# Kernel tuning notes

Hardware: AMD Instinct MI355X
Metric: run time of the kernel (lower is better)

Reference implementation:

```python
import jax, jax.numpy as jnp
import numpy as np

K = 5            # neighbors
TEMP = 1.0       # softmax temperature
BANK = 1000      # fixed bank capacity in source
B = 65536        # batch
D = 256          # feature_dim
EPS = 1e-12      # F.normalize eps


def _l2norm(x):
    # F.normalize(x, dim=1): x / max(||x||, eps)
    n = jnp.sqrt(jnp.sum(x * x, axis=1, keepdims=True))
    return x / jnp.maximum(n, EPS)


def setup_inputs() -> dict:
    key = jax.random.key(0)
    k1, k2, k3, k4 = jax.random.split(key, 4)
    features = jax.random.normal(k1, (B, D), dtype=jnp.float32)
    feature_bank = jax.random.normal(k2, (BANK, D), dtype=jnp.float32)
    # fusion_layer: Linear(2D -> D), ReLU, Linear(D -> D). torch weight layout [out, in].
    W1 = jax.random.normal(k3, (D, 2 * D), dtype=jnp.float32) * (1.0 / np.sqrt(2 * D))
    b1 = jnp.zeros((D,), dtype=jnp.float32)
    W2 = jax.random.normal(k4, (D, D), dtype=jnp.float32) * (1.0 / np.sqrt(D))
    b2 = jnp.zeros((D,), dtype=jnp.float32)
    return {"features": features, "feature_bank": feature_bank,
            "W1": W1, "b1": b1, "W2": W2, "b2": b2}


def reference(features, feature_bank, W1, b1, W2, b2):
    # knn_search: cosine similarity against the (full) bank
    qn = _l2norm(features)                      # [B, D]
    bn = _l2norm(feature_bank)                  # [BANK, D]
    sims = qn @ bn.T                            # [B, BANK]
    top_s, top_i = jax.lax.top_k(sims, K)       # [B, K]
    w = jax.nn.softmax(top_s / TEMP, axis=1)    # [B, K]
    neigh = feature_bank[top_i]                 # gather -> [B, K, D]
    nf = jnp.einsum('bkd,bk->bd', neigh, w)     # weighted average of neighbors
    # fusion MLP on concat([query, neighbors])
    fused = jnp.concatenate([features, nf], axis=1)    # [B, 2D]
    h = jax.nn.relu(fused @ W1.T + b1)                 # [B, D]
    out = h @ W2.T + b2                                # [B, D]
    return out
```

## Files before the change

kernel.cpp:

```cpp
#include <hip/hip_runtime.h>

#define DIM 256
#define NC 12

typedef __attribute__((ext_vector_type(8))) short short8;
typedef __attribute__((ext_vector_type(4))) float f32x4;

__device__ __forceinline__ short f32bf(float f) {
    unsigned u = __builtin_bit_cast(unsigned, f);
    unsigned r = u + 0x7FFFu + ((u >> 16) & 1u);
    return (short)(r >> 16);
}

template<int CTRL>
__device__ __forceinline__ unsigned dppmax(unsigned x) {
    unsigned y = (unsigned)__builtin_amdgcn_update_dpp(0, (int)x, CTRL, 0xF, 0xF, true);
    return x > y ? x : y;
}

__global__ __launch_bounds__(256) void k_prep(const float* __restrict__ bank,
        const float* __restrict__ W1, const float* __restrict__ W2,
        short* __restrict__ bnbf, double* __restrict__ binv,
        short* __restrict__ w1bf, short* __restrict__ w2bf)
{
    __shared__ double part[4];
    __shared__ double s_inv;
    const int bid = blockIdx.x, t = threadIdx.x;
    if (bid < 1024) {
        const int row = bid;
        if (row < 1000) {
            float v = bank[(size_t)row * DIM + t];
            double ssq = (double)v * (double)v;
            for (int o = 32; o > 0; o >>= 1) ssq += __shfl_down(ssq, o);
            if ((t & 63) == 0) part[t >> 6] = ssq;
            __syncthreads();
            if (t == 0) {
                double s = part[0] + part[1] + part[2] + part[3];
                double n = sqrt(s); if (n < 1e-12) n = 1e-12;
                double inv = 1.0 / n;
                binv[row] = inv; s_inv = inv;
            }
            __syncthreads();
            bnbf[(size_t)row * DIM + t] = f32bf((float)((double)v * s_inv));
        } else {
            bnbf[(size_t)row * DIM + t] = 0;
            if (t == 0) binv[row] = 0.0;
        }
    } else if (bid < 1536) {
        const int i = (bid - 1024) * 256 + t;
        w1bf[i] = f32bf(W1[i]);
    } else {
        const int i = (bid - 1536) * 256 + t;
        w2bf[i] = f32bf(W2[i]);
    }
}

__global__ __launch_bounds__(256) void k_sims(const float* __restrict__ feat,
        const short* __restrict__ bnbf, int* __restrict__ top)
{
    __shared__ alignas(16) short S[32 * 1032];
    const int t = threadIdx.x, lane = t & 63, w = t >> 6;
    const int n16 = lane & 15, q4 = lane >> 4;
    const int qb = blockIdx.x * 32;

    short8 bq[8][2];
    #pragma unroll
    for (int kc = 0; kc < 8; ++kc)
        #pragma unroll
        for (int nt = 0; nt < 2; ++nt) {
            const float4* s = (const float4*)(feat + (size_t)(qb + nt * 16 + n16) * DIM + kc * 32 + q4 * 8);
            float4 v0 = s[0], v1 = s[1];
            short8 f;
            f[0] = f32bf(v0.x); f[1] = f32bf(v0.y); f[2] = f32bf(v0.z); f[3] = f32bf(v0.w);
            f[4] = f32bf(v1.x); f[5] = f32bf(v1.y); f[6] = f32bf(v1.z); f[7] = f32bf(v1.w);
            bq[kc][nt] = f;
        }

    const char* Abase = (const char*)bnbf + ((size_t)(w * 16 + n16) * DIM + q4 * 8) * 2;
    const f32x4 vzero = {0.f, 0.f, 0.f, 0.f};

    short8 A[3][8];
    #pragma unroll
    for (int kc = 0; kc < 8; ++kc) A[0][kc] = *(const short8*)(Abase + kc * 64);
    #pragma unroll
    for (int kc = 0; kc < 8; ++kc) A[1][kc] = *(const short8*)(Abase + 32768 + kc * 64);

    #pragma unroll
    for (int chunk = 0; chunk < 16; ++chunk) {
        if (chunk + 2 < 16) {
            const char* nb = Abase + (size_t)(chunk + 2) * 32768;
            #pragma unroll
            for (int kc = 0; kc < 8; ++kc)
                A[(chunk + 2) % 3][kc] = *(const short8*)(nb + kc * 64);
        }
        f32x4 acc0 = vzero, acc1 = vzero;
        #pragma unroll
        for (int kc = 0; kc < 8; ++kc) {
            acc0 = __builtin_amdgcn_mfma_f32_16x16x32_bf16(A[chunk % 3][kc], bq[kc][0], acc0, 0, 0, 0);
            acc1 = __builtin_amdgcn_mfma_f32_16x16x32_bf16(A[chunk % 3][kc], bq[kc][1], acc1, 0, 0, 0);
        }
        const int bankb = chunk * 64 + w * 16 + q4 * 4;
        {
            uint2 u;
            u.x = ((unsigned)(unsigned short)f32bf(acc0[0])) |
                  (((unsigned)(unsigned short)f32bf(acc0[1])) << 16);
            u.y = ((unsigned)(unsigned short)f32bf(acc0[2])) |
                  (((unsigned)(unsigned short)f32bf(acc0[3])) << 16);
            *(uint2*)(S + (size_t)n16 * 1032 + bankb) = u;
            u.x = ((unsigned)(unsigned short)f32bf(acc1[0])) |
                  (((unsigned)(unsigned short)f32bf(acc1[1])) << 16);
            u.y = ((unsigned)(unsigned short)f32bf(acc1[2])) |
                  (((unsigned)(unsigned short)f32bf(acc1[3])) << 16);
            *(uint2*)(S + (size_t)(16 + n16) * 1032 + bankb) = u;
        }
    }
    __syncthreads();

    for (int i = 0; i < 8; ++i) {
        const int ql = w * 8 + i;
        const uint4* p = (const uint4*)(S + (size_t)ql * 1032 + lane * 16);
        uint4 a = p[0], b = p[1];

        unsigned k[16];
        {
            unsigned words[8] = {a.x, a.y, a.z, a.w, b.x, b.y, b.z, b.w};
            #pragma unroll
            for (int j = 0; j < 16; ++j) {
                unsigned h = (j & 1) ? (words[j >> 1] >> 16) : (words[j >> 1] & 0xFFFFu);
                unsigned m = (h ^ 0x8000u) ^ ((0u - (h >> 15)) & 0x7FFFu);
                int idx = lane * 16 + j;
                k[j] = (idx < 1000) ? ((m << 16) | (unsigned)idx) : 0u;
            }
        }
        #pragma unroll
        for (int sz = 2; sz <= 16; sz <<= 1)
            #pragma unroll
            for (int st = sz >> 1; st >= 1; st >>= 1)
                #pragma unroll
                for (int ii = 0; ii < 16; ++ii) {
                    int j = ii ^ st;
                    if (j > ii) {
                        bool desc = ((ii & sz) == 0);
                        unsigned lo = k[ii], hi = k[j];
                        unsigned mx = lo > hi ? lo : hi;
                        unsigned mn = lo > hi ? hi : lo;
                        k[ii] = desc ? mx : mn;
                        k[j] = desc ? mn : mx;
                    }
                }
        unsigned mine = 0;
        #pragma unroll
        for (int r = 0; r < 12; ++r) {
            unsigned m = k[0];
            m = dppmax<0xB1>(m);
            m = dppmax<0x4E>(m);
            m = dppmax<0x141>(m);
            m = dppmax<0x140>(m);
            m = dppmax<0x142>(m);
            m = dppmax<0x143>(m);
            unsigned wm = (unsigned)__builtin_amdgcn_readlane((int)m, 63);
            if (lane == r) mine = wm;
            if (k[0] == wm) {
                #pragma unroll
                for (int s = 0; s < 12; ++s) k[s] = k[s + 1];
            }
        }
        if (lane < 12) top[(size_t)(qb + ql) * NC + lane] = (int)(mine & 0xFFFFu);
    }
}

__global__ __launch_bounds__(256) void k_refine(const float* __restrict__ feat,
        const float* __restrict__ bank, const int* __restrict__ top,
        const double* __restrict__ binv, short* __restrict__ nf,
        short* __restrict__ featbf)
{
    __shared__ int    cidxL[16 * NC];
    __shared__ float  bdF[16 * NC];
    __shared__ double bdD[16 * NC];
    __shared__ float  simsF[16 * NC];
    __shared__ double simsD[16 * NC];
    __shared__ float  qiL[16];
    __shared__ int    flagL[16];
    __shared__ int    selidx[16][5];
    __shared__ float  selw[16][5];

    const int t = threadIdx.x, lane = t & 63, w = t >> 6;
    const int g = lane >> 4, u = lane & 15;
    const int ql = w * 4 + g;
    const int qbase = blockIdx.x * 16;
    const int q = qbase + ql;

    if (t < 16 * NC) {
        const int c = top[(size_t)qbase * NC + t];
        cidxL[t] = c;
        const double b = binv[c];
        bdD[t] = b; bdF[t] = (float)b;
    }
    __syncthreads();

    int ci[NC];
    #pragma unroll
    for (int c = 0; c < NC; ++c) ci[c] = cidxL[ql * NC + c];

    float qf[16];
    float ssf = 0.f;
    #pragma unroll
    for (int j = 0; j < 4; ++j) {
        float4 v = *(const float4*)(feat + (size_t)q * DIM + j * 64 + u * 4);
        qf[j*4+0] = v.x; qf[j*4+1] = v.y; qf[j*4+2] = v.z; qf[j*4+3] = v.w;
        ssf += v.x*v.x + v.y*v.y + v.z*v.z + v.w*v.w;
    }
    {
        short* fb = featbf + (size_t)q * DIM + u * 4;
        #pragma unroll
        for (int j = 0; j < 4; ++j) {
            uint2 pk;
            pk.x = ((unsigned)(unsigned short)f32bf(qf[j*4+0])) |
                   (((unsigned)(unsigned short)f32bf(qf[j*4+1])) << 16);
            pk.y = ((unsigned)(unsigned short)f32bf(qf[j*4+2])) |
                   (((unsigned)(unsigned short)f32bf(qf[j*4+3])) << 16);
            *(uint2*)(fb + j * 64) = pk;
        }
    }
    #pragma unroll
    for (int o = 1; o < 16; o <<= 1) ssf += __shfl_xor(ssf, o, 16);
    float nq = sqrtf(ssf); if (nq < 1e-12f) nq = 1e-12f;
    if (u == 0) qiL[ql] = 1.f / nq;

    float s[NC];
    #pragma unroll
    for (int c = 0; c < NC; ++c) {
        const float* brow = bank + (size_t)ci[c] * DIM + u * 4;
        float a0 = 0.f, a1 = 0.f, a2 = 0.f, a3 = 0.f;
        #pragma unroll
        for (int j = 0; j < 4; ++j) {
            float4 b = *(const float4*)(brow + j * 64);
            a0 += qf[j*4+0] * b.x; a1 += qf[j*4+1] * b.y;
            a2 += qf[j*4+2] * b.z; a3 += qf[j*4+3] * b.w;
        }
        s[c] = (a0 + a1) + (a2 + a3);
    }
    #pragma unroll
    for (int o = 1; o < 16; o <<= 1)
        #pragma unroll
        for (int c = 0; c < NC; ++c) s[c] += __shfl_xor(s[c], o, 16);
    #pragma unroll
    for (int c = 0; c < NC; ++c) if (u == c) simsF[ql * NC + c] = s[c];
    __syncthreads();

    if (t < 16) {
        const float qi2 = qiL[t];
        float vf[NC];
        unsigned long long key[NC];
        int cid[NC];
        #pragma unroll
        for (int c = 0; c < NC; ++c) {
            cid[c] = cidxL[t * NC + c];
            float v = simsF[t * NC + c] * qi2 * bdF[t * NC + c];
            vf[c] = v;
            unsigned ub = __builtin_bit_cast(unsigned, v);
            unsigned m = (ub >> 31) ? ~ub : (ub | 0x80000000u);
            key[c] = ((unsigned long long)m << 10) | (unsigned long long)(1023 - cid[c]);
        }
        int rank[NC];
        #pragma unroll
        for (int c = 0; c < NC; ++c) rank[c] = 0;
        #pragma unroll
        for (int c1 = 0; c1 < NC; ++c1)
            #pragma unroll
            for (int c2 = c1 + 1; c2 < NC; ++c2) {
                const bool gt = key[c1] > key[c2];
                rank[c2] += gt ? 1 : 0;
                rank[c1] += gt ? 0 : 1;
            }
        float v5 = 0.f, v6 = 0.f;
        #pragma unroll
        for (int c = 0; c < NC; ++c) {
            v5 += (rank[c] == 4) ? vf[c] : 0.f;
            v6 += (rank[c] == 5) ? vf[c] : 0.f;
        }
        flagL[t] = (v5 - v6) < 2e-6f;

        float vm = vf[0];
        #pragma unroll
        for (int c = 1; c < NC; ++c) vm = fmaxf(vm, vf[c]);
        float e[NC]; float wsum = 0.f;
        #pragma unroll
        for (int c = 0; c < NC; ++c) {
            float ex = __expf(vf[c] - vm);
            ex = (rank[c] < 5) ? ex : 0.f;
            e[c] = ex; wsum += ex;
        }
        const float inv = 1.f / wsum;
        #pragma unroll
        for (int k = 0; k < 5; ++k) {
            int idx = 0; float wv = 0.f;
            #pragma unroll
            for (int c = 0; c < NC; ++c) {
                const bool is = (rank[c] == k);
                idx += is ? cid[c] : 0;
                wv  += is ? e[c]  : 0.f;
            }
            selidx[t][k] = idx; selw[t][k] = wv * inv;
        }
    }
    __syncthreads();

    if (flagL[ql]) {
        double ssd = 0.0;
        #pragma unroll
        for (int j = 0; j < 16; ++j) ssd += (double)qf[j] * (double)qf[j];
        #pragma unroll
        for (int o = 1; o < 16; o <<= 1) ssd += __shfl_xor(ssd, o, 16);
        double nd = sqrt(ssd); if (nd < 1e-12) nd = 1e-12;
        const double qid = 1.0 / nd;
        double sd[NC];
        #pragma unroll
        for (int c = 0; c < NC; ++c) {
            const float* brow = bank + (size_t)ci[c] * DIM + u * 4;
            double a0 = 0, a1 = 0, a2 = 0, a3 = 0;
            #pragma unroll
            for (int j = 0; j < 4; ++j) {
                float4 b = *(const float4*)(brow + j * 64);
                a0 += (double)qf[j*4+0] * b.x; a1 += (double)qf[j*4+1] * b.y;
                a2 += (double)qf[j*4+2] * b.z; a3 += (double)qf[j*4+3] * b.w;
            }
            sd[c] = (a0 + a1) + (a2 + a3);
        }
        #pragma unroll
        for (int o = 1; o < 16; o <<= 1)
            #pragma unroll
            for (int c = 0; c < NC; ++c) sd[c] += __shfl_xor(sd[c], o, 16);
        #pragma unroll
        for (int c = 0; c < NC; ++c)
            if (u == c) simsD[ql * NC + c] = sd[c] * qid * bdD[ql * NC + c];
    }
    __syncthreads();

    if (t < 16 && flagL[t]) {
        double vd[NC];
        unsigned long long key[NC];
        int cid[NC];
        #pragma unroll
        for (int c = 0; c < NC; ++c) {
            cid[c] = cidxL[t * NC + c];
            double v = simsD[t * NC + c];
            vd[c] = v;
            unsigned long long ub = __builtin_bit_cast(unsigned long long, v);
            unsigned long long m = (ub >> 63) ? ~ub : (ub | 0x8000000000000000ULL);
            key[c] = (m & ~0x3FFULL) | (unsigned long long)(1023 - cid[c]);
        }
        int rank[NC];
        #pragma unroll
        for (int c = 0; c < NC; ++c) rank[c] = 0;
        #pragma unroll
        for (int c1 = 0; c1 < NC; ++c1)
            #pragma unroll
            for (int c2 = c1 + 1; c2 < NC; ++c2) {
                const bool gt = key[c1] > key[c2];
                rank[c2] += gt ? 1 : 0;
                rank[c1] += gt ? 0 : 1;
            }
        float vf[NC];
        #pragma unroll
        for (int c = 0; c < NC; ++c) vf[c] = (float)vd[c];
        float vm = vf[0];
        #pragma unroll
        for (int c = 1; c < NC; ++c) vm = fmaxf(vm, vf[c]);
        float e[NC]; float wsum = 0.f;
        #pragma unroll
        for (int c = 0; c < NC; ++c) {
            float ex = __expf(vf[c] - vm);
            ex = (rank[c] < 5) ? ex : 0.f;
            e[c] = ex; wsum += ex;
        }
        const float inv = 1.f / wsum;
        #pragma unroll
        for (int k = 0; k < 5; ++k) {
            int idx = 0; float wv = 0.f;
            #pragma unroll
            for (int c = 0; c < NC; ++c) {
                const bool is = (rank[c] == k);
                idx += is ? cid[c] : 0;
                wv  += is ? e[c]  : 0.f;
            }
            selidx[t][k] = idx; selw[t][k] = wv * inv;
        }
    }
    __syncthreads();

    float wk[5]; int ik[5];
    #pragma unroll
    for (int k = 0; k < 5; ++k) { wk[k] = selw[ql][k]; ik[k] = selidx[ql][k]; }
    float4 oa[4];
    #pragma unroll
    for (int j = 0; j < 4; ++j) { oa[j].x = 0.f; oa[j].y = 0.f; oa[j].z = 0.f; oa[j].w = 0.f; }
    #pragma unroll
    for (int k = 0; k < 5; ++k) {
        const float wc = wk[k];
        const float* brow = bank + (size_t)ik[k] * DIM + u * 4;
        #pragma unroll
        for (int j = 0; j < 4; ++j) {
            float4 b = *(const float4*)(brow + j * 64);
            oa[j].x += wc * b.x; oa[j].y += wc * b.y;
            oa[j].z += wc * b.z; oa[j].w += wc * b.w;
        }
    }
    short* od = nf + (size_t)q * DIM + u * 4;
    #pragma unroll
    for (int j = 0; j < 4; ++j) {
        uint2 pk;
        pk.x = ((unsigned)(unsigned short)f32bf(oa[j].x)) |
               (((unsigned)(unsigned short)f32bf(oa[j].y)) << 16);
        pk.y = ((unsigned)(unsigned short)f32bf(oa[j].z)) |
               (((unsigned)(unsigned short)f32bf(oa[j].w)) << 16);
        *(uint2*)(od + j * 64) = pk;
    }
}

__global__ __launch_bounds__(256, 4) void k_mlp(const short* __restrict__ featbf,
        const short* __restrict__ nf, const short* __restrict__ w1bf,
        const short* __restrict__ w2bf, const float* __restrict__ b1,
        const float* __restrict__ b2, float* __restrict__ out)
{
    __shared__ alignas(16) short Hs[64 * 264];
    const int t = threadIdx.x, lane = t & 63, w = t >> 6;
    const int mb = blockIdx.x * 64;
    const int n16 = lane & 15, ko = (lane >> 4) << 3;
    const int rq = (lane >> 4) << 2, cc = lane & 15;
    const f32x4 vzero = {0.f, 0.f, 0.f, 0.f};

    f32x4 acc[4][4];
    #pragma unroll
    for (int a = 0; a < 4; ++a)
        #pragma unroll
        for (int b = 0; b < 4; ++b) acc[a][b] = vzero;

    const short* A0 = featbf + (size_t)mb * 256 + ko;
    const short* A1 = nf     + (size_t)mb * 256 + ko;
    const short* Wp = w1bf + (size_t)(w * 64 + n16) * 512 + ko;

    #pragma unroll
    for (int kc = 0; kc < 8; ++kc) {
        short8 af[4], bf[4];
        #pragma unroll
        for (int mt = 0; mt < 4; ++mt)
            af[mt] = *(const short8*)(A0 + (mt * 16 + n16) * 256 + kc * 32);
        #pragma unroll
        for (int nt = 0; nt < 4; ++nt)
            bf[nt] = *(const short8*)(Wp + (size_t)nt * 16 * 512 + kc * 32);
        #pragma unroll
        for (int mt = 0; mt < 4; ++mt)
            #pragma unroll
            for (int nt = 0; nt < 4; ++nt)
                acc[mt][nt] = __builtin_amdgcn_mfma_f32_16x16x32_bf16(af[mt], bf[nt], acc[mt][nt], 0, 0, 0);
    }
    #pragma unroll
    for (int kc = 0; kc < 8; ++kc) {
        short8 af[4], bf[4];
        #pragma unroll
        for (int mt = 0; mt < 4; ++mt)
            af[mt] = *(const short8*)(A1 + (mt * 16 + n16) * 256 + kc * 32);
        #pragma unroll
        for (int nt = 0; nt < 4; ++nt)
            bf[nt] = *(const short8*)(Wp + (size_t)nt * 16 * 512 + (kc + 8) * 32);
        #pragma unroll
        for (int mt = 0; mt < 4; ++mt)
            #pragma unroll
            for (int nt = 0; nt < 4; ++nt)
                acc[mt][nt] = __builtin_amdgcn_mfma_f32_16x16x32_bf16(af[mt], bf[nt], acc[mt][nt], 0, 0, 0);
    }

    #pragma unroll
    for (int mt = 0; mt < 4; ++mt)
        #pragma unroll
        for (int nt = 0; nt < 4; ++nt) {
            const int row = mt * 16 + rq;
            const int col = w * 64 + nt * 16 + cc;
            const float bias = b1[col];
            #pragma unroll
            for (int rr = 0; rr < 4; ++rr) {
                float v = acc[mt][nt][rr] + bias;
                Hs[(row + rr) * 264 + col] = f32bf(fmaxf(v, 0.f));
            }
        }
    #pragma unroll
    for (int a = 0; a < 4; ++a)
        #pragma unroll
        for (int b = 0; b < 4; ++b) acc[a][b] = vzero;
    __syncthreads();

    #pragma unroll
    for (int kc = 0; kc < 8; ++kc) {
        short8 bf[4];
        #pragma unroll
        for (int nt = 0; nt < 4; ++nt)
            bf[nt] = *(const short8*)(w2bf + (size_t)(w * 64 + nt * 16 + n16) * 256 + kc * 32 + ko);
        short8 af[4];
        #pragma unroll
        for (int mt = 0; mt < 4; ++mt)
            af[mt] = *(const short8*)(Hs + (mt * 16 + n16) * 264 + kc * 32 + ko);
        #pragma unroll
        for (int mt = 0; mt < 4; ++mt)
            #pragma unroll
            for (int nt = 0; nt < 4; ++nt)
                acc[mt][nt] = __builtin_amdgcn_mfma_f32_16x16x32_bf16(af[mt], bf[nt], acc[mt][nt], 0, 0, 0);
    }
    #pragma unroll
    for (int mt = 0; mt < 4; ++mt)
        #pragma unroll
        for (int nt = 0; nt < 4; ++nt) {
            const int row = mb + mt * 16 + rq;
            const int col = w * 64 + nt * 16 + cc;
            const float bias = b2[col];
            #pragma unroll
            for (int rr = 0; rr < 4; ++rr)
                out[(size_t)(row + rr) * 256 + col] = acc[mt][nt][rr] + bias;
        }
}

extern "C" void kernel_launch(void* const* d_in, const int* in_sizes, int n_in,
                              void* d_out, int out_size, void* d_ws, size_t ws_size,
                              hipStream_t stream) {
    const float* feat = (const float*)d_in[0];
    const float* bank = (const float*)d_in[1];
    const float* W1   = (const float*)d_in[2];
    const float* b1   = (const float*)d_in[3];
    const float* W2   = (const float*)d_in[4];
    const float* b2   = (const float*)d_in[5];
    float* out = (float*)d_out;

    char* ws = (char*)d_ws;
    short*  bnbf = (short*)(ws + 0);
    double* binv = (double*)(ws + 524288);
    short*  w1bf = (short*)(ws + 532480);
    short*  w2bf = (short*)(ws + 794624);
    int*    top  = (int*)(ws + 925696);
    short*  nf   = (short*)(ws + 4071424);
    short*  featbf = (short*)(ws + 37625856);

    k_prep<<<1792, 256, 0, stream>>>(bank, W1, W2, bnbf, binv, w1bf, w2bf);
    k_sims<<<2048, 256, 0, stream>>>(feat, bnbf, top);
    k_refine<<<4096, 256, 0, stream>>>(feat, bank, top, binv, nf, featbf);
    k_mlp  <<<1024, 256, 0, stream>>>(featbf, nf, w1bf, w2bf, b1, b2, out);
}
```

Measured before the change: 391.6 us.

## Halve k_sims query tile to 16 and move bf16 feature conversion into it

Each k_sims block now handles 16 queries instead of 32, which halves shared memory and register use and doubles the grid, with launch bounds requesting 4 blocks per CU. The bf16 conversion of the features, already done in k_sims for the MFMA operands, is now also written to featbf there, so k_refine no longer repeats it. The trade-off is that each block streams the whole bf16 bank for half as many queries, doubling bank traffic through the cache, in exchange for more parallelism and shorter top-k loops per wave.

```diff
diff --git a/kernel.cpp b/kernel.cpp
--- a/kernel.cpp
+++ b/kernel.cpp
@@ -55,26 +55,30 @@
     }
 }
 
-__global__ __launch_bounds__(256) void k_sims(const float* __restrict__ feat,
-        const short* __restrict__ bnbf, int* __restrict__ top)
+__global__ __launch_bounds__(256, 4) void k_sims(const float* __restrict__ feat,
+        const short* __restrict__ bnbf, int* __restrict__ top,
+        short* __restrict__ featbf)
 {
-    __shared__ alignas(16) short S[32 * 1032];
+    __shared__ alignas(16) short S[16 * 1032];
     const int t = threadIdx.x, lane = t & 63, w = t >> 6;
     const int n16 = lane & 15, q4 = lane >> 4;
-    const int qb = blockIdx.x * 32;
-
-    short8 bq[8][2];
-    #pragma unroll
-    for (int kc = 0; kc < 8; ++kc)
-        #pragma unroll
-        for (int nt = 0; nt < 2; ++nt) {
-            const float4* s = (const float4*)(feat + (size_t)(qb + nt * 16 + n16) * DIM + kc * 32 + q4 * 8);
-            float4 v0 = s[0], v1 = s[1];
-            short8 f;
-            f[0] = f32bf(v0.x); f[1] = f32bf(v0.y); f[2] = f32bf(v0.z); f[3] = f32bf(v0.w);
-            f[4] = f32bf(v1.x); f[5] = f32bf(v1.y); f[6] = f32bf(v1.z); f[7] = f32bf(v1.w);
-            bq[kc][nt] = f;
-        }
+    const int qb = blockIdx.x * 16;
+
+    short8 bq[8];
+    #pragma unroll
+    for (int kc = 0; kc < 8; ++kc) {
+        const float4* s = (const float4*)(feat + (size_t)(qb + n16) * DIM + kc * 32 + q4 * 8);
+        float4 v0 = s[0], v1 = s[1];
+        short8 f;
+        f[0] = f32bf(v0.x); f[1] = f32bf(v0.y); f[2] = f32bf(v0.z); f[3] = f32bf(v0.w);
+        f[4] = f32bf(v1.x); f[5] = f32bf(v1.y); f[6] = f32bf(v1.z); f[7] = f32bf(v1.w);
+        bq[kc] = f;
+    }
+    if (w == 0) {
+        #pragma unroll
+        for (int kc = 0; kc < 8; ++kc)
+            *(short8*)(featbf + (size_t)(qb + n16) * DIM + kc * 32 + q4 * 8) = bq[kc];
+    }
 
     const char* Abase = (const char*)bnbf + ((size_t)(w * 16 + n16) * DIM + q4 * 8) * 2;
     const f32x4 vzero = {0.f, 0.f, 0.f, 0.f};
@@ -93,31 +97,22 @@
             for (int kc = 0; kc < 8; ++kc)
                 A[(chunk + 2) % 3][kc] = *(const short8*)(nb + kc * 64);
         }
-        f32x4 acc0 = vzero, acc1 = vzero;
-        #pragma unroll
-        for (int kc = 0; kc < 8; ++kc) {
-            acc0 = __builtin_amdgcn_mfma_f32_16x16x32_bf16(A[chunk % 3][kc], bq[kc][0], acc0, 0, 0, 0);
-            acc1 = __builtin_amdgcn_mfma_f32_16x16x32_bf16(A[chunk % 3][kc], bq[kc][1], acc1, 0, 0, 0);
-        }
+        f32x4 acc = vzero;
+        #pragma unroll
+        for (int kc = 0; kc < 8; ++kc)
+            acc = __builtin_amdgcn_mfma_f32_16x16x32_bf16(A[chunk % 3][kc], bq[kc], acc, 0, 0, 0);
         const int bankb = chunk * 64 + w * 16 + q4 * 4;
-        {
-            uint2 u;
-            u.x = ((unsigned)(unsigned short)f32bf(acc0[0])) |
-                  (((unsigned)(unsigned short)f32bf(acc0[1])) << 16);
-            u.y = ((unsigned)(unsigned short)f32bf(acc0[2])) |
-                  (((unsigned)(unsigned short)f32bf(acc0[3])) << 16);
-            *(uint2*)(S + (size_t)n16 * 1032 + bankb) = u;
-            u.x = ((unsigned)(unsigned short)f32bf(acc1[0])) |
-                  (((unsigned)(unsigned short)f32bf(acc1[1])) << 16);
-            u.y = ((unsigned)(unsigned short)f32bf(acc1[2])) |
-                  (((unsigned)(unsigned short)f32bf(acc1[3])) << 16);
-            *(uint2*)(S + (size_t)(16 + n16) * 1032 + bankb) = u;
-        }
-    }
-    __syncthreads();
-
-    for (int i = 0; i < 8; ++i) {
-        const int ql = w * 8 + i;
+        uint2 u;
+        u.x = ((unsigned)(unsigned short)f32bf(acc[0])) |
+              (((unsigned)(unsigned short)f32bf(acc[1])) << 16);
+        u.y = ((unsigned)(unsigned short)f32bf(acc[2])) |
+              (((unsigned)(unsigned short)f32bf(acc[3])) << 16);
+        *(uint2*)(S + (size_t)n16 * 1032 + bankb) = u;
+    }
+    __syncthreads();
+
+    for (int i = 0; i < 4; ++i) {
+        const int ql = w * 4 + i;
         const uint4* p = (const uint4*)(S + (size_t)ql * 1032 + lane * 16);
         uint4 a = p[0], b = p[1];
 
@@ -171,8 +166,7 @@
 
 __global__ __launch_bounds__(256) void k_refine(const float* __restrict__ feat,
         const float* __restrict__ bank, const int* __restrict__ top,
-        const double* __restrict__ binv, short* __restrict__ nf,
-        short* __restrict__ featbf)
+        const double* __restrict__ binv, short* __restrict__ nf)
 {
     __shared__ int    cidxL[16 * NC];
     __shared__ float  bdF[16 * NC];
@@ -209,18 +203,6 @@
         float4 v = *(const float4*)(feat + (size_t)q * DIM + j * 64 + u * 4);
         qf[j*4+0] = v.x; qf[j*4+1] = v.y; qf[j*4+2] = v.z; qf[j*4+3] = v.w;
         ssf += v.x*v.x + v.y*v.y + v.z*v.z + v.w*v.w;
-    }
-    {
-        short* fb = featbf + (size_t)q * DIM + u * 4;
-        #pragma unroll
-        for (int j = 0; j < 4; ++j) {
-            uint2 pk;
-            pk.x = ((unsigned)(unsigned short)f32bf(qf[j*4+0])) |
-                   (((unsigned)(unsigned short)f32bf(qf[j*4+1])) << 16);
-            pk.y = ((unsigned)(unsigned short)f32bf(qf[j*4+2])) |
-                   (((unsigned)(unsigned short)f32bf(qf[j*4+3])) << 16);
-            *(uint2*)(fb + j * 64) = pk;
-        }
     }
     #pragma unroll
     for (int o = 1; o < 16; o <<= 1) ssf += __shfl_xor(ssf, o, 16);
@@ -540,7 +522,7 @@
     short*  featbf = (short*)(ws + 37625856);
 
     k_prep<<<1792, 256, 0, stream>>>(bank, W1, W2, bnbf, binv, w1bf, w2bf);
-    k_sims<<<2048, 256, 0, stream>>>(feat, bnbf, top);
-    k_refine<<<4096, 256, 0, stream>>>(feat, bank, top, binv, nf, featbf);
+    k_sims<<<4096, 256, 0, stream>>>(feat, bnbf, top, featbf);
+    k_refine<<<4096, 256, 0, stream>>>(feat, bank, top, binv, nf);
     k_mlp  <<<1024, 256, 0, stream>>>(featbf, nf, w1bf, w2bf, b1, b2, out);
 }
```

Result: slower. 537.8 us (+37.4%).

## Compute top-k selection redundantly per lane group and move bf16 feature write to k_sims

Applied to the files above, without the earlier changes.

In k_refine, every lane of each 16-lane group now computes the rank selection, softmax and the double-precision recheck redundantly in registers. Previously only 16 threads did this work, using shared memory staging and several block-wide barriers. The bf16 conversion of the query features is now written by k_sims, which already converts them, so k_refine no longer does that store. The cost is more redundant ALU work and register pressure in k_refine, plus extra global stores in k_sims.

```diff
diff --git a/kernel.cpp b/kernel.cpp
--- a/kernel.cpp
+++ b/kernel.cpp
@@ -56,7 +56,8 @@
 }
 
 __global__ __launch_bounds__(256) void k_sims(const float* __restrict__ feat,
-        const short* __restrict__ bnbf, int* __restrict__ top)
+        const short* __restrict__ bnbf, int* __restrict__ top,
+        short* __restrict__ featbf)
 {
     __shared__ alignas(16) short S[32 * 1032];
     const int t = threadIdx.x, lane = t & 63, w = t >> 6;
@@ -75,6 +76,13 @@
             f[4] = f32bf(v1.x); f[5] = f32bf(v1.y); f[6] = f32bf(v1.z); f[7] = f32bf(v1.w);
             bq[kc][nt] = f;
         }
+    if (w == 0) {
+        #pragma unroll
+        for (int kc = 0; kc < 8; ++kc)
+            #pragma unroll
+            for (int nt = 0; nt < 2; ++nt)
+                *(short8*)(featbf + (size_t)(qb + nt * 16 + n16) * DIM + kc * 32 + q4 * 8) = bq[kc][nt];
+    }
 
     const char* Abase = (const char*)bnbf + ((size_t)(w * 16 + n16) * DIM + q4 * 8) * 2;
     const f32x4 vzero = {0.f, 0.f, 0.f, 0.f};
@@ -171,18 +179,11 @@
 
 __global__ __launch_bounds__(256) void k_refine(const float* __restrict__ feat,
         const float* __restrict__ bank, const int* __restrict__ top,
-        const double* __restrict__ binv, short* __restrict__ nf,
-        short* __restrict__ featbf)
+        const double* __restrict__ binv, short* __restrict__ nf)
 {
     __shared__ int    cidxL[16 * NC];
     __shared__ float  bdF[16 * NC];
     __shared__ double bdD[16 * NC];
-    __shared__ float  simsF[16 * NC];
-    __shared__ double simsD[16 * NC];
-    __shared__ float  qiL[16];
-    __shared__ int    flagL[16];
-    __shared__ int    selidx[16][5];
-    __shared__ float  selw[16][5];
 
     const int t = threadIdx.x, lane = t & 63, w = t >> 6;
     const int g = lane >> 4, u = lane & 15;
@@ -210,22 +211,10 @@
         qf[j*4+0] = v.x; qf[j*4+1] = v.y; qf[j*4+2] = v.z; qf[j*4+3] = v.w;
         ssf += v.x*v.x + v.y*v.y + v.z*v.z + v.w*v.w;
     }
-    {
-        short* fb = featbf + (size_t)q * DIM + u * 4;
-        #pragma unroll
-        for (int j = 0; j < 4; ++j) {
-            uint2 pk;
-            pk.x = ((unsigned)(unsigned short)f32bf(qf[j*4+0])) |
-                   (((unsigned)(unsigned short)f32bf(qf[j*4+1])) << 16);
-            pk.y = ((unsigned)(unsigned short)f32bf(qf[j*4+2])) |
-                   (((unsigned)(unsigned short)f32bf(qf[j*4+3])) << 16);
-            *(uint2*)(fb + j * 64) = pk;
-        }
-    }
     #pragma unroll
     for (int o = 1; o < 16; o <<= 1) ssf += __shfl_xor(ssf, o, 16);
     float nq = sqrtf(ssf); if (nq < 1e-12f) nq = 1e-12f;
-    if (u == 0) qiL[ql] = 1.f / nq;
+    const float qi2 = 1.f / nq;
 
     float s[NC];
     #pragma unroll
@@ -244,23 +233,19 @@
     for (int o = 1; o < 16; o <<= 1)
         #pragma unroll
         for (int c = 0; c < NC; ++c) s[c] += __shfl_xor(s[c], o, 16);
-    #pragma unroll
-    for (int c = 0; c < NC; ++c) if (u == c) simsF[ql * NC + c] = s[c];
-    __syncthreads();
-
-    if (t < 16) {
-        const float qi2 = qiL[t];
+
+    float selwR[5]; int selidxR[5];
+    bool flag;
+    {
         float vf[NC];
         unsigned long long key[NC];
-        int cid[NC];
         #pragma unroll
         for (int c = 0; c < NC; ++c) {
-            cid[c] = cidxL[t * NC + c];
-            float v = simsF[t * NC + c] * qi2 * bdF[t * NC + c];
+            float v = s[c] * qi2 * bdF[ql * NC + c];
             vf[c] = v;
             unsigned ub = __builtin_bit_cast(unsigned, v);
             unsigned m = (ub >> 31) ? ~ub : (ub | 0x80000000u);
-            key[c] = ((unsigned long long)m << 10) | (unsigned long long)(1023 - cid[c]);
+            key[c] = ((unsigned long long)m << 10) | (unsigned long long)(1023 - ci[c]);
         }
         int rank[NC];
         #pragma unroll
@@ -279,7 +264,7 @@
             v5 += (rank[c] == 4) ? vf[c] : 0.f;
             v6 += (rank[c] == 5) ? vf[c] : 0.f;
         }
-        flagL[t] = (v5 - v6) < 2e-6f;
+        flag = (v5 - v6) < 2e-6f;
 
         float vm = vf[0];
         #pragma unroll
@@ -298,15 +283,14 @@
             #pragma unroll
             for (int c = 0; c < NC; ++c) {
                 const bool is = (rank[c] == k);
-                idx += is ? cid[c] : 0;
+                idx += is ? ci[c] : 0;
                 wv  += is ? e[c]  : 0.f;
             }
-            selidx[t][k] = idx; selw[t][k] = wv * inv;
-        }
-    }
-    __syncthreads();
-
-    if (flagL[ql]) {
+            selidxR[k] = idx; selwR[k] = wv * inv;
+        }
+    }
+
+    if (flag) {
         double ssd = 0.0;
         #pragma unroll
         for (int j = 0; j < 16; ++j) ssd += (double)qf[j] * (double)qf[j];
@@ -331,24 +315,16 @@
         for (int o = 1; o < 16; o <<= 1)
             #pragma unroll
             for (int c = 0; c < NC; ++c) sd[c] += __shfl_xor(sd[c], o, 16);
-        #pragma unroll
-        for (int c = 0; c < NC; ++c)
-            if (u == c) simsD[ql * NC + c] = sd[c] * qid * bdD[ql * NC + c];
-    }
-    __syncthreads();
-
-    if (t < 16 && flagL[t]) {
+
         double vd[NC];
         unsigned long long key[NC];
-        int cid[NC];
         #pragma unroll
         for (int c = 0; c < NC; ++c) {
-            cid[c] = cidxL[t * NC + c];
-            double v = simsD[t * NC + c];
+            double v = sd[c] * qid * bdD[ql * NC + c];
             vd[c] = v;
             unsigned long long ub = __builtin_bit_cast(unsigned long long, v);
             unsigned long long m = (ub >> 63) ? ~ub : (ub | 0x8000000000000000ULL);
-            key[c] = (m & ~0x3FFULL) | (unsigned long long)(1023 - cid[c]);
+            key[c] = (m & ~0x3FFULL) | (unsigned long long)(1023 - ci[c]);
         }
         int rank[NC];
         #pragma unroll
@@ -381,24 +357,20 @@
             #pragma unroll
             for (int c = 0; c < NC; ++c) {
                 const bool is = (rank[c] == k);
-                idx += is ? cid[c] : 0;
+                idx += is ? ci[c] : 0;
                 wv  += is ? e[c]  : 0.f;
             }
-            selidx[t][k] = idx; selw[t][k] = wv * inv;
-        }
-    }
-    __syncthreads();
-
-    float wk[5]; int ik[5];
-    #pragma unroll
-    for (int k = 0; k < 5; ++k) { wk[k] = selw[ql][k]; ik[k] = selidx[ql][k]; }
+            selidxR[k] = idx; selwR[k] = wv * inv;
+        }
+    }
+
     float4 oa[4];
     #pragma unroll
     for (int j = 0; j < 4; ++j) { oa[j].x = 0.f; oa[j].y = 0.f; oa[j].z = 0.f; oa[j].w = 0.f; }
     #pragma unroll
     for (int k = 0; k < 5; ++k) {
-        const float wc = wk[k];
-        const float* brow = bank + (size_t)ik[k] * DIM + u * 4;
+        const float wc = selwR[k];
+        const float* brow = bank + (size_t)selidxR[k] * DIM + u * 4;
         #pragma unroll
         for (int j = 0; j < 4; ++j) {
             float4 b = *(const float4*)(brow + j * 64);
@@ -540,7 +512,7 @@
     short*  featbf = (short*)(ws + 37625856);
 
     k_prep<<<1792, 256, 0, stream>>>(bank, W1, W2, bnbf, binv, w1bf, w2bf);
-    k_sims<<<2048, 256, 0, stream>>>(feat, bnbf, top);
-    k_refine<<<4096, 256, 0, stream>>>(feat, bank, top, binv, nf, featbf);
+    k_sims<<<2048, 256, 0, stream>>>(feat, bnbf, top, featbf);
+    k_refine<<<4096, 256, 0, stream>>>(feat, bank, top, binv, nf);
     k_mlp  <<<1024, 256, 0, stream>>>(featbf, nf, w1bf, w2bf, b1, b2, out);
 }
```

After: 439.9 us. +12.3%, slower.
